# Performance work log

Hardware: AMD Instinct MI355X
Metric: run time of the kernel (lower is better)

## Reference

```python
import jax, jax.numpy as jnp
import numpy as np


def setup_inputs() -> dict:
    key = jax.random.key(0)
    ks = jax.random.split(key, 4)
    B, T, M, E, F = 4, 2048, 1024, 8, 4096
    hidden_states = jax.random.normal(ks[0], (B, T, M), dtype=jnp.float32)
    wg = jax.random.normal(ks[1], (M, E), dtype=jnp.float32) * (1.0 / np.sqrt(M))
    w1 = jax.random.normal(ks[2], (E, M, F), dtype=jnp.float32) * (1.0 / np.sqrt(M))
    b1 = jnp.zeros((E, F), dtype=jnp.float32)
    w2 = jax.random.normal(ks[3], (E, F, M), dtype=jnp.float32) * (1.0 / np.sqrt(F))
    b2 = jnp.zeros((E, M), dtype=jnp.float32)
    return {"hidden_states": hidden_states, "wg": wg, "w1": w1, "b1": b1, "w2": w2, "b2": b2}


def reference(hidden_states, wg, w1, b1, w2, b2):
    B, T, M = hidden_states.shape
    E = wg.shape[1]
    S = B * T
    MIN_CAPACITY = 4
    C = max((S + E - 1) // E, MIN_CAPACITY)  # capacity_factor = 1 (static)

    x = hidden_states.reshape(S, M)  # [S, M]

    # --- top-1 gating (deepspeed TopKGate, noisy=None, use_rts=False) ---
    logits = x @ wg                                  # [S, E]
    gates = jax.nn.softmax(logits, axis=-1)          # [S, E]
    idx = jnp.argmax(gates, axis=-1)                 # [S]
    mask1 = jax.nn.one_hot(idx, E, dtype=gates.dtype)  # [S, E]
    # aux loss (computed before capacity drop)
    l_aux = jnp.sum(gates.mean(0) * mask1.mean(0)) * E
    # position of each token within its expert's queue
    locations1 = jnp.cumsum(mask1, axis=0) - 1.0     # [S, E]
    mask1 = mask1 * (locations1 < C)                 # drop overflow tokens
    gates1_s = jnp.sum(gates * mask1, axis=1)        # [S]
    loc_s = jnp.sum(locations1 * mask1, axis=1).astype(jnp.int32)  # [S]
    loc_sc = jax.nn.one_hot(loc_s, C, dtype=gates.dtype)           # [S, C]

    combine_weights = jnp.einsum('se,sc->sec', gates1_s[:, None] * mask1, loc_sc)  # [S,E,C]
    dispatch_mask = (combine_weights > 0).astype(x.dtype)

    # --- dispatch ---
    dispatched = jnp.einsum('sec,sm->ecm', dispatch_mask, x)  # [E, C, M]

    # --- expert FFN (grouped GEMM) ---
    h = jax.nn.gelu(jnp.einsum('ecm,emf->ecf', dispatched, w1) + b1[:, None, :])
    expert_out = jnp.einsum('ecf,efm->ecm', h, w2) + b2[:, None, :]  # [E, C, M]

    # --- combine ---
    out = jnp.einsum('sec,ecm->sm', combine_weights, expert_out)  # [S, M]
    return out.reshape(B, T, M)
```

## Files before the change

kernel.cpp:

```cpp
#include <hip/hip_runtime.h>
#include <hip/hip_bf16.h>
#include <math.h>

#define S_TOK 8192
#define M_DIM 1024
#define E_NUM 8
#define F_DIM 4096
#define CAP   1024

typedef short short8 __attribute__((ext_vector_type(8)));
typedef float f32x4 __attribute__((ext_vector_type(4)));
typedef unsigned short ushortx4 __attribute__((ext_vector_type(4)));

__device__ inline unsigned short f2bf(float f) {
    union { float f; unsigned int u; } v; v.f = f;
    unsigned int r = v.u + 0x7fffu + ((v.u >> 16) & 1u);
    return (unsigned short)(r >> 16);
}

__device__ inline float gelu_fast(float x) {
    float y = 0.7978845608028654f * (x + 0.044715f * x * x * x);
    if (y > 40.f) return x;
    float e = exp2f(2.8853900817779268f * y);
    return x * e / (e + 1.0f);
}

__device__ inline void gl_lds16(const void* g, void* l) {
    __builtin_amdgcn_global_load_lds(
        (const __attribute__((address_space(1))) unsigned int*)g,
        (__attribute__((address_space(3))) unsigned int*)l, 16, 0, 0);
}

__global__ __launch_bounds__(256) void gating_kernel(
    const float* __restrict__ x, const float* __restrict__ wg,
    int* __restrict__ idx, float* __restrict__ gate)
{
    int wid = threadIdx.x >> 6;
    int lane = threadIdx.x & 63;
    int s = blockIdx.x * 4 + wid;
    const float* xs = x + (size_t)s * M_DIM;

    double acc[E_NUM];
#pragma unroll
    for (int e = 0; e < E_NUM; e++) acc[e] = 0.0;

    for (int i = lane; i < M_DIM; i += 64) {
        float xv = xs[i];
        float4 wa = *(const float4*)(wg + (size_t)i * E_NUM);
        float4 wb = *(const float4*)(wg + (size_t)i * E_NUM + 4);
        acc[0] += (double)xv * (double)wa.x;
        acc[1] += (double)xv * (double)wa.y;
        acc[2] += (double)xv * (double)wa.z;
        acc[3] += (double)xv * (double)wa.w;
        acc[4] += (double)xv * (double)wb.x;
        acc[5] += (double)xv * (double)wb.y;
        acc[6] += (double)xv * (double)wb.z;
        acc[7] += (double)xv * (double)wb.w;
    }
#pragma unroll
    for (int e = 0; e < E_NUM; e++) {
        double v = acc[e];
        for (int o = 32; o > 0; o >>= 1) v += __shfl_down(v, o, 64);
        acc[e] = v;
    }
    if (lane == 0) {
        double mx = acc[0]; int am = 0;
#pragma unroll
        for (int e = 1; e < E_NUM; e++) {
            if (acc[e] > mx) { mx = acc[e]; am = e; }
        }
        double se = 0.0;
#pragma unroll
        for (int e = 0; e < E_NUM; e++) se += exp(acc[e] - mx);
        idx[s] = am;
        gate[s] = (float)(1.0 / se);
    }
}

__global__ __launch_bounds__(1024) void scan_build(
    const int* __restrict__ idx, int* __restrict__ srcmap)
{
    __shared__ unsigned int sc[2][4][1024];
    int t = threadIdx.x;

    for (int i = t; i < E_NUM * CAP; i += 1024) srcmap[i] = -1;

    int eid[8];
    unsigned int cnt[E_NUM];
#pragma unroll
    for (int e = 0; e < E_NUM; e++) cnt[e] = 0;
#pragma unroll
    for (int i = 0; i < 8; i++) {
        int e = idx[t * 8 + i];
        eid[i] = e;
        cnt[e]++;
    }
    unsigned int pk[4];
#pragma unroll
    for (int i = 0; i < 4; i++) pk[i] = cnt[2 * i] | (cnt[2 * i + 1] << 16);
#pragma unroll
    for (int i = 0; i < 4; i++) sc[0][i][t] = pk[i];

    int buf = 0;
    for (int ofs = 1; ofs < 1024; ofs <<= 1) {
        __syncthreads();
        unsigned int v[4];
#pragma unroll
        for (int i = 0; i < 4; i++) {
            v[i] = sc[buf][i][t] + ((t >= ofs) ? sc[buf][i][t - ofs] : 0u);
            sc[buf ^ 1][i][t] = v[i];
        }
        buf ^= 1;
    }
    __syncthreads();
    unsigned int pos[E_NUM];
#pragma unroll
    for (int e = 0; e < E_NUM; e++) {
        unsigned int incl = (sc[buf][e >> 1][t] >> ((e & 1) * 16)) & 0xffffu;
        pos[e] = incl - cnt[e];
    }
#pragma unroll
    for (int i = 0; i < 8; i++) {
        int e = eid[i];
        unsigned int p = pos[e]++;
        if (p < CAP) srcmap[e * CAP + p] = t * 8 + i;
    }
}

__global__ __launch_bounds__(256) void dispatch_kernel(
    const float* __restrict__ x, const int* __restrict__ srcmap,
    unsigned short* __restrict__ A1)
{
    int slot = blockIdx.x;
    int s = srcmap[slot];
    int t = threadIdx.x;
    ushortx4 o;
    if (s >= 0) {
        float4 v = ((const float4*)(x + (size_t)s * M_DIM))[t];
        o[0] = f2bf(v.x); o[1] = f2bf(v.y); o[2] = f2bf(v.z); o[3] = f2bf(v.w);
    } else {
        o[0] = 0; o[1] = 0; o[2] = 0; o[3] = 0;
    }
    ((ushortx4*)(A1 + (size_t)slot * M_DIM))[t] = o;
}

__global__ __launch_bounds__(256) void transpose_cvt(
    const float* __restrict__ in, unsigned short* __restrict__ out, int R, int Cc)
{
    __shared__ float tile[32][33];
    int e = blockIdx.z;
    int br = blockIdx.y * 32, bc = blockIdx.x * 32;
    const float* ine = in + (size_t)e * R * Cc;
    unsigned short* oute = out + (size_t)e * R * Cc;
    int tx = threadIdx.x, ty = threadIdx.y;
#pragma unroll
    for (int i = 0; i < 32; i += 8)
        tile[ty + i][tx] = ine[(size_t)(br + ty + i) * Cc + (bc + tx)];
    __syncthreads();
#pragma unroll
    for (int i = 0; i < 32; i += 8)
        oute[(size_t)(bc + ty + i) * R + (br + tx)] = f2bf(tile[tx][ty + i]);
}

template <int MODE>
__global__ __launch_bounds__(256) void gemm_bf16(
    const unsigned short* __restrict__ A, const unsigned short* __restrict__ B,
    const float* __restrict__ bias, float* __restrict__ OutF,
    unsigned short* __restrict__ OutH,
    const int* __restrict__ srcmap, const float* __restrict__ gate,
    int K, int RA, int NB, int tilesM, int tilesN)
{
    __shared__ __align__(16) unsigned short As[2][128 * 32];
    __shared__ __align__(16) unsigned short Bs[2][128 * 32];

    int bid = blockIdx.x;
    int tpe = tilesM * tilesN;
    int e = bid / tpe;
    int rem = bid - e * tpe;
    int tm = rem / tilesN;
    int tn = rem - tm * tilesN;

    const unsigned short* Ae = A + ((size_t)e * RA + (size_t)tm * 128) * K;
    const unsigned short* Be = B + ((size_t)e * NB + (size_t)tn * 128) * K;

    int tid = threadIdx.x;
    int wid = tid >> 6, lane = tid & 63;
    int srow = wid * 32 + (lane >> 2);
    int schunk = (lane & 3) * 8;

    int fr = lane & 15, fk = (lane >> 4) * 8;
    int r0 = (wid >> 1) * 64, c0 = (wid & 1) * 64;

#define STAGE(bufi, kk) do {                                                  \
    const unsigned short* ga = Ae + (size_t)srow * K + (kk) + schunk;         \
    const unsigned short* gb = Be + (size_t)srow * K + (kk) + schunk;         \
    gl_lds16(ga,                 &As[bufi][srow * 32 + schunk]);              \
    gl_lds16(ga + (size_t)16 * K, &As[bufi][(srow + 16) * 32 + schunk]);      \
    gl_lds16(gb,                 &Bs[bufi][srow * 32 + schunk]);              \
    gl_lds16(gb + (size_t)16 * K, &Bs[bufi][(srow + 16) * 32 + schunk]);      \
} while (0)

    f32x4 acc[4][4];
#pragma unroll
    for (int i = 0; i < 4; i++)
#pragma unroll
        for (int j = 0; j < 4; j++) acc[i][j] = (f32x4){0.f, 0.f, 0.f, 0.f};

    STAGE(0, 0);
    asm volatile("s_waitcnt vmcnt(0)" ::: "memory");
    __syncthreads();

    int cur = 0;
    for (int k0 = 0; k0 < K; k0 += 32) {
        if (k0 + 32 < K) STAGE(cur ^ 1, k0 + 32);

        short8 a[4], b[4];
#pragma unroll
        for (int mi = 0; mi < 4; mi++)
            a[mi] = *(const short8*)&As[cur][(r0 + mi * 16 + fr) * 32 + fk];
#pragma unroll
        for (int ni = 0; ni < 4; ni++)
            b[ni] = *(const short8*)&Bs[cur][(c0 + ni * 16 + fr) * 32 + fk];
#pragma unroll
        for (int mi = 0; mi < 4; mi++)
#pragma unroll
            for (int ni = 0; ni < 4; ni++)
                acc[mi][ni] = __builtin_amdgcn_mfma_f32_16x16x32_bf16(
                    a[mi], b[ni], acc[mi][ni], 0, 0, 0);

        asm volatile("s_waitcnt vmcnt(0)" ::: "memory");
        __syncthreads();
        cur ^= 1;
    }
#undef STAGE

    int orow = (lane >> 4) * 4, ocol = lane & 15;
    if (MODE == 0) {
#pragma unroll
        for (int mi = 0; mi < 4; mi++) {
#pragma unroll
            for (int j = 0; j < 4; j++) {
                int r = tm * 128 + r0 + mi * 16 + orow + j;
                size_t rowbase = ((size_t)e * RA + r) * NB;
#pragma unroll
                for (int ni = 0; ni < 4; ni++) {
                    int c = tn * 128 + c0 + ni * 16 + ocol;
                    float v = acc[mi][ni][j] + bias[e * NB + c];
                    OutH[rowbase + c] = f2bf(gelu_fast(v));
                }
            }
        }
    } else {
#pragma unroll
        for (int mi = 0; mi < 4; mi++) {
#pragma unroll
            for (int j = 0; j < 4; j++) {
                int r = tm * 128 + r0 + mi * 16 + orow + j;
                int slot = e * RA + r;
                int s = srcmap[slot];
                if (s < 0) continue;
                float g = gate[s];
                size_t rowbase = (size_t)s * NB;
#pragma unroll
                for (int ni = 0; ni < 4; ni++) {
                    int c = tn * 128 + c0 + ni * 16 + ocol;
                    OutF[rowbase + c] = g * (acc[mi][ni][j] + bias[e * NB + c]);
                }
            }
        }
    }
}

extern "C" void kernel_launch(void* const* d_in, const int* in_sizes, int n_in,
                              void* d_out, int out_size, void* d_ws, size_t ws_size,
                              hipStream_t stream) {
    const float* x  = (const float*)d_in[0];
    const float* wg = (const float*)d_in[1];
    const float* w1 = (const float*)d_in[2];
    const float* b1 = (const float*)d_in[3];
    const float* w2 = (const float*)d_in[4];
    const float* b2 = (const float*)d_in[5];
    float* out = (float*)d_out;

    char* ws = (char*)d_ws;
    unsigned short* A1  = (unsigned short*)(ws);
    unsigned short* W1T = (unsigned short*)(ws + (size_t)(16u << 20));
    unsigned short* W2T = (unsigned short*)(ws + (size_t)(80u << 20));
    unsigned short* H   = (unsigned short*)(ws + (size_t)(144u << 20));
    int*   idx  = (int*)(ws + (size_t)(208u << 20));
    float* gate = (float*)(ws + (size_t)(208u << 20) + 32768);
    int*   srcm = (int*)(ws + (size_t)(208u << 20) + 65536);

    hipMemsetAsync(d_out, 0, (size_t)S_TOK * M_DIM * sizeof(float), stream);

    gating_kernel<<<S_TOK / 4, 256, 0, stream>>>(x, wg, idx, gate);
    scan_build<<<1, 1024, 0, stream>>>(idx, srcm);
    dispatch_kernel<<<E_NUM * CAP, 256, 0, stream>>>(x, srcm, A1);
    transpose_cvt<<<dim3(F_DIM / 32, M_DIM / 32, E_NUM), dim3(32, 8), 0, stream>>>(
        w1, W1T, M_DIM, F_DIM);
    transpose_cvt<<<dim3(M_DIM / 32, F_DIM / 32, E_NUM), dim3(32, 8), 0, stream>>>(
        w2, W2T, F_DIM, M_DIM);

    gemm_bf16<0><<<E_NUM * (CAP / 128) * (F_DIM / 128), 256, 0, stream>>>(
        A1, W1T, b1, nullptr, H, nullptr, nullptr,
        M_DIM, CAP, F_DIM, CAP / 128, F_DIM / 128);

    gemm_bf16<1><<<E_NUM * (CAP / 128) * (M_DIM / 128), 256, 0, stream>>>(
        H, W2T, b2, out, nullptr, srcm, gate,
        F_DIM, CAP, M_DIM, CAP / 128, M_DIM / 128);
}
```

Before: 375.8 us.

## Use 256x256 tiles with 4-stage LDS pipeline and split-K second GEMM

Replaces the 128x128 double-buffered bf16 GEMM with a 256x256 tile, 512-thread kernel that uses a 4-slot LDS ring with partial vmcnt waits, swizzled LDS layout, workgroup index swizzling, and MFMA priority hints. The second GEMM is split along K into two halves that write fp32 partials into workspace, and a new combine kernel sums the partials, adds bias, scales by gate and scatters to output. This aims to raise arithmetic intensity, hide load latency and fill the GPU for the smaller second GEMM, at the cost of an extra partial buffer round trip and one more launch. P overlays the W1T workspace region, which is safe only because W1T is no longer needed by then.

```diff
diff --git a/kernel.cpp b/kernel.cpp
--- a/kernel.cpp
+++ b/kernel.cpp
@@ -163,112 +163,157 @@
 }
 
 template <int MODE>
-__global__ __launch_bounds__(256) void gemm_bf16(
+__global__ __launch_bounds__(512, 1) void gemm256(
     const unsigned short* __restrict__ A, const unsigned short* __restrict__ B,
-    const float* __restrict__ bias, float* __restrict__ OutF,
-    unsigned short* __restrict__ OutH,
-    const int* __restrict__ srcmap, const float* __restrict__ gate,
-    int K, int RA, int NB, int tilesM, int tilesN)
-{
-    __shared__ __align__(16) unsigned short As[2][128 * 32];
-    __shared__ __align__(16) unsigned short Bs[2][128 * 32];
+    const float* __restrict__ bias, unsigned short* __restrict__ OutH,
+    float* __restrict__ OutP)
+{
+    constexpr int K   = (MODE == 0) ? 1024 : 4096;
+    constexpr int NB  = (MODE == 0) ? 4096 : 1024;
+    constexpr int NT  = (MODE == 0) ? 32 : 64;
+    constexpr int NWG = (MODE == 0) ? 512 : 256;
+
+    __shared__ unsigned short Asm[4 * 8192];
+    __shared__ unsigned short Bsm[4 * 8192];
 
     int bid = blockIdx.x;
-    int tpe = tilesM * tilesN;
-    int e = bid / tpe;
-    int rem = bid - e * tpe;
-    int tm = rem / tilesN;
-    int tn = rem - tm * tilesN;
-
-    const unsigned short* Ae = A + ((size_t)e * RA + (size_t)tm * 128) * K;
-    const unsigned short* Be = B + ((size_t)e * NB + (size_t)tn * 128) * K;
+    int swz = (bid & 7) * (NWG / 8) + (bid >> 3);
+    int e, tm, tn, ks, kOff;
+    if (MODE == 0) {
+        e = swz >> 6; int rem = swz & 63; tm = rem >> 4; tn = rem & 15; ks = 0; kOff = 0;
+    } else {
+        ks = swz & 1; int q = swz >> 1; e = q >> 4; int rem = q & 15;
+        tm = rem >> 2; tn = rem & 3; kOff = ks * 2048;
+    }
+
+    const unsigned short* Ae = A + ((size_t)e * CAP + (size_t)tm * 256) * K;
+    const unsigned short* Be = B + ((size_t)e * NB + (size_t)tn * 256) * K;
 
     int tid = threadIdx.x;
     int wid = tid >> 6, lane = tid & 63;
-    int srow = wid * 32 + (lane >> 2);
-    int schunk = (lane & 3) * 8;
-
-    int fr = lane & 15, fk = (lane >> 4) * 8;
-    int r0 = (wid >> 1) * 64, c0 = (wid & 1) * 64;
-
-#define STAGE(bufi, kk) do {                                                  \
-    const unsigned short* ga = Ae + (size_t)srow * K + (kk) + schunk;         \
-    const unsigned short* gb = Be + (size_t)srow * K + (kk) + schunk;         \
-    gl_lds16(ga,                 &As[bufi][srow * 32 + schunk]);              \
-    gl_lds16(ga + (size_t)16 * K, &As[bufi][(srow + 16) * 32 + schunk]);      \
-    gl_lds16(gb,                 &Bs[bufi][srow * 32 + schunk]);              \
-    gl_lds16(gb + (size_t)16 * K, &Bs[bufi][(srow + 16) * 32 + schunk]);      \
-} while (0)
-
-    f32x4 acc[4][4];
-#pragma unroll
-    for (int i = 0; i < 4; i++)
+    int wm = wid >> 2, wn = wid & 3;
+    int fr = lane & 15, kq = lane >> 4;
+    int swc = ((kq ^ ((fr >> 1) & 3)) << 3);
+
+    int rr = tid >> 2;
+    int cg = (tid & 3) ^ ((rr >> 1) & 3);
+    const unsigned short* srcA0 = Ae + (size_t)rr * K + kOff + cg * 8;
+    const unsigned short* srcA1 = srcA0 + (size_t)128 * K;
+    const unsigned short* srcB0 = Be + (size_t)rr * K + kOff + cg * 8;
+    const unsigned short* srcB1 = srcB0 + (size_t)128 * K;
+    unsigned short* ldsA = Asm + wid * 512;
+    unsigned short* ldsB = Bsm + wid * 512;
+
+#define STG_A(t_) do { int sl_ = ((t_) & 3) * 8192; int kk_ = (t_) * 32;          \
+    gl_lds16(srcA0 + kk_, ldsA + sl_); gl_lds16(srcA1 + kk_, ldsA + sl_ + 4096); } while (0)
+#define STG_B(t_) do { int sl_ = ((t_) & 3) * 8192; int kk_ = (t_) * 32;          \
+    gl_lds16(srcB0 + kk_, ldsB + sl_); gl_lds16(srcB1 + kk_, ldsB + sl_ + 4096); } while (0)
+
+    f32x4 acc[8][4];
+#pragma unroll
+    for (int i = 0; i < 8; i++)
 #pragma unroll
         for (int j = 0; j < 4; j++) acc[i][j] = (f32x4){0.f, 0.f, 0.f, 0.f};
 
-    STAGE(0, 0);
-    asm volatile("s_waitcnt vmcnt(0)" ::: "memory");
-    __syncthreads();
-
-    int cur = 0;
-    for (int k0 = 0; k0 < K; k0 += 32) {
-        if (k0 + 32 < K) STAGE(cur ^ 1, k0 + 32);
-
+    STG_A(0); STG_B(0); STG_A(1); STG_B(1); STG_A(2); STG_B(2);
+
+    int arow = wm * 128 + fr;
+    int brow = wn * 64 + fr;
+
+    for (int t = 0; t < NT; ++t) {
+        int sl = (t & 3) * 8192;
+        int rem = NT - 1 - t;
+        if (rem > 1)       asm volatile("s_waitcnt vmcnt(8)" ::: "memory");
+        else if (rem == 1) asm volatile("s_waitcnt vmcnt(4)" ::: "memory");
+        else               asm volatile("s_waitcnt vmcnt(0)" ::: "memory");
+        asm volatile("s_barrier" ::: "memory");
+
+        if (t + 3 < NT) STG_A(t + 3);
         short8 a[4], b[4];
 #pragma unroll
         for (int mi = 0; mi < 4; mi++)
-            a[mi] = *(const short8*)&As[cur][(r0 + mi * 16 + fr) * 32 + fk];
+            a[mi] = *(const short8*)&Asm[sl + (arow + mi * 16) * 32 + swc];
 #pragma unroll
         for (int ni = 0; ni < 4; ni++)
-            b[ni] = *(const short8*)&Bs[cur][(c0 + ni * 16 + fr) * 32 + fk];
+            b[ni] = *(const short8*)&Bsm[sl + (brow + ni * 16) * 32 + swc];
+        __builtin_amdgcn_s_setprio(1);
 #pragma unroll
         for (int mi = 0; mi < 4; mi++)
 #pragma unroll
             for (int ni = 0; ni < 4; ni++)
                 acc[mi][ni] = __builtin_amdgcn_mfma_f32_16x16x32_bf16(
                     a[mi], b[ni], acc[mi][ni], 0, 0, 0);
-
-        asm volatile("s_waitcnt vmcnt(0)" ::: "memory");
-        __syncthreads();
-        cur ^= 1;
-    }
-#undef STAGE
-
-    int orow = (lane >> 4) * 4, ocol = lane & 15;
+        __builtin_amdgcn_s_setprio(0);
+
+        if (t + 3 < NT) STG_B(t + 3);
+#pragma unroll
+        for (int mi = 0; mi < 4; mi++)
+            a[mi] = *(const short8*)&Asm[sl + (arow + (mi + 4) * 16) * 32 + swc];
+        __builtin_amdgcn_s_setprio(1);
+#pragma unroll
+        for (int mi = 0; mi < 4; mi++)
+#pragma unroll
+            for (int ni = 0; ni < 4; ni++)
+                acc[mi + 4][ni] = __builtin_amdgcn_mfma_f32_16x16x32_bf16(
+                    a[mi], b[ni], acc[mi + 4][ni], 0, 0, 0);
+        __builtin_amdgcn_s_setprio(0);
+    }
+#undef STG_A
+#undef STG_B
+
+    int orow = kq * 4, ocol = fr;
+    int cbase = tn * 256 + wn * 64;
     if (MODE == 0) {
-#pragma unroll
-        for (int mi = 0; mi < 4; mi++) {
+        float bv[4];
+#pragma unroll
+        for (int ni = 0; ni < 4; ni++) bv[ni] = bias[e * NB + cbase + ni * 16 + ocol];
+#pragma unroll
+        for (int mi = 0; mi < 8; mi++) {
 #pragma unroll
             for (int j = 0; j < 4; j++) {
-                int r = tm * 128 + r0 + mi * 16 + orow + j;
-                size_t rowbase = ((size_t)e * RA + r) * NB;
-#pragma unroll
-                for (int ni = 0; ni < 4; ni++) {
-                    int c = tn * 128 + c0 + ni * 16 + ocol;
-                    float v = acc[mi][ni][j] + bias[e * NB + c];
-                    OutH[rowbase + c] = f2bf(gelu_fast(v));
-                }
+                int r = tm * 256 + wm * 128 + mi * 16 + orow + j;
+                size_t rowbase = ((size_t)e * CAP + r) * NB + cbase;
+#pragma unroll
+                for (int ni = 0; ni < 4; ni++)
+                    OutH[rowbase + ni * 16 + ocol] = f2bf(gelu_fast(acc[mi][ni][j] + bv[ni]));
             }
         }
     } else {
-#pragma unroll
-        for (int mi = 0; mi < 4; mi++) {
+        float* OP = OutP + (size_t)ks * S_TOK * M_DIM;
+#pragma unroll
+        for (int mi = 0; mi < 8; mi++) {
 #pragma unroll
             for (int j = 0; j < 4; j++) {
-                int r = tm * 128 + r0 + mi * 16 + orow + j;
-                int slot = e * RA + r;
-                int s = srcmap[slot];
-                if (s < 0) continue;
-                float g = gate[s];
-                size_t rowbase = (size_t)s * NB;
-#pragma unroll
-                for (int ni = 0; ni < 4; ni++) {
-                    int c = tn * 128 + c0 + ni * 16 + ocol;
-                    OutF[rowbase + c] = g * (acc[mi][ni][j] + bias[e * NB + c]);
-                }
+                int r = tm * 256 + wm * 128 + mi * 16 + orow + j;
+                size_t rowbase = ((size_t)e * CAP + r) * NB + cbase;
+#pragma unroll
+                for (int ni = 0; ni < 4; ni++)
+                    OP[rowbase + ni * 16 + ocol] = acc[mi][ni][j];
             }
         }
     }
+}
+
+__global__ __launch_bounds__(256) void combine_kernel(
+    const float* __restrict__ P, const int* __restrict__ srcmap,
+    const float* __restrict__ gate, const float* __restrict__ b2,
+    float* __restrict__ out)
+{
+    int r = blockIdx.x;
+    int s = srcmap[r];
+    if (s < 0) return;
+    int e = r >> 10;
+    float g = gate[s];
+    int t = threadIdx.x;
+    float4 p0 = ((const float4*)P)[r * 256 + t];
+    float4 p1 = ((const float4*)(P + (size_t)S_TOK * M_DIM))[r * 256 + t];
+    float4 bb = ((const float4*)b2)[e * 256 + t];
+    float4 o;
+    o.x = g * (p0.x + p1.x + bb.x);
+    o.y = g * (p0.y + p1.y + bb.y);
+    o.z = g * (p0.z + p1.z + bb.z);
+    o.w = g * (p0.w + p1.w + bb.w);
+    ((float4*)out)[s * 256 + t] = o;
 }
 
 extern "C" void kernel_launch(void* const* d_in, const int* in_sizes, int n_in,
@@ -285,6 +330,7 @@
     char* ws = (char*)d_ws;
     unsigned short* A1  = (unsigned short*)(ws);
     unsigned short* W1T = (unsigned short*)(ws + (size_t)(16u << 20));
+    float*          P   = (float*)(ws + (size_t)(16u << 20));
     unsigned short* W2T = (unsigned short*)(ws + (size_t)(80u << 20));
     unsigned short* H   = (unsigned short*)(ws + (size_t)(144u << 20));
     int*   idx  = (int*)(ws + (size_t)(208u << 20));
@@ -301,11 +347,9 @@
     transpose_cvt<<<dim3(M_DIM / 32, F_DIM / 32, E_NUM), dim3(32, 8), 0, stream>>>(
         w2, W2T, F_DIM, M_DIM);
 
-    gemm_bf16<0><<<E_NUM * (CAP / 128) * (F_DIM / 128), 256, 0, stream>>>(
-        A1, W1T, b1, nullptr, H, nullptr, nullptr,
-        M_DIM, CAP, F_DIM, CAP / 128, F_DIM / 128);
-
-    gemm_bf16<1><<<E_NUM * (CAP / 128) * (M_DIM / 128), 256, 0, stream>>>(
-        H, W2T, b2, out, nullptr, srcm, gate,
-        F_DIM, CAP, M_DIM, CAP / 128, M_DIM / 128);
-}
+    gemm256<0><<<512, 512, 0, stream>>>(A1, W1T, b1, H, nullptr);
+
+    gemm256<1><<<256, 512, 0, stream>>>(H, W2T, nullptr, nullptr, P);
+
+    combine_kernel<<<E_NUM * CAP, 256, 0, stream>>>(P, srcm, gate, b2, out);
+}
```

New measurement: 341.8 us. 1.1x faster.

## Rewrite expert GEMMs with larger tiles, swizzled LDS and staged epilogue

Applied to the files above, without the earlier changes.

Replaces the 128x128x32 bf16 GEMM with a 512-thread kernel using 256x256 (FFN1) or 128x256 (FFN2) tiles and a K-step of 64. LDS rows get an XOR swizzle to avoid bank conflicts, and blocks are remapped for cache locality. MFMA issue is bracketed with setprio, and the FFN1 epilogue writes through LDS so global stores are vectorised. The goal is more data reuse per tile and fewer barriers per K; the cost is higher register and LDS pressure, which may lower occupancy.

```diff
diff --git a/kernel.cpp b/kernel.cpp
--- a/kernel.cpp
+++ b/kernel.cpp
@@ -163,109 +163,163 @@
 }
 
 template <int MODE>
-__global__ __launch_bounds__(256) void gemm_bf16(
+__global__ __launch_bounds__(512) void gemm256(
     const unsigned short* __restrict__ A, const unsigned short* __restrict__ B,
-    const float* __restrict__ bias, float* __restrict__ OutF,
-    unsigned short* __restrict__ OutH,
-    const int* __restrict__ srcmap, const float* __restrict__ gate,
-    int K, int RA, int NB, int tilesM, int tilesN)
-{
-    __shared__ __align__(16) unsigned short As[2][128 * 32];
-    __shared__ __align__(16) unsigned short Bs[2][128 * 32];
+    const float* __restrict__ bias, unsigned short* __restrict__ OutH,
+    float* __restrict__ OutF, const int* __restrict__ srcmap,
+    const float* __restrict__ gate)
+{
+    constexpr int K    = (MODE == 0) ? 1024 : 4096;
+    constexpr int NB   = (MODE == 0) ? 4096 : 1024;
+    constexpr int BM   = (MODE == 0) ? 256 : 128;
+    constexpr int NT   = K / 64;
+    constexpr int NWG  = (MODE == 0) ? 512 : 256;
+    constexpr int AI   = BM / 64;
+    constexpr int MI   = BM / 32;
+    constexpr int ASLOT = BM * 64;
+    constexpr int BBASE = BM * 128;
+
+    __shared__ __align__(16) unsigned short LDS[BBASE + 32768];
 
     int bid = blockIdx.x;
-    int tpe = tilesM * tilesN;
-    int e = bid / tpe;
-    int rem = bid - e * tpe;
-    int tm = rem / tilesN;
-    int tn = rem - tm * tilesN;
-
-    const unsigned short* Ae = A + ((size_t)e * RA + (size_t)tm * 128) * K;
-    const unsigned short* Be = B + ((size_t)e * NB + (size_t)tn * 128) * K;
-
-    int tid = threadIdx.x;
-    int wid = tid >> 6, lane = tid & 63;
-    int srow = wid * 32 + (lane >> 2);
-    int schunk = (lane & 3) * 8;
-
-    int fr = lane & 15, fk = (lane >> 4) * 8;
-    int r0 = (wid >> 1) * 64, c0 = (wid & 1) * 64;
-
-#define STAGE(bufi, kk) do {                                                  \
-    const unsigned short* ga = Ae + (size_t)srow * K + (kk) + schunk;         \
-    const unsigned short* gb = Be + (size_t)srow * K + (kk) + schunk;         \
-    gl_lds16(ga,                 &As[bufi][srow * 32 + schunk]);              \
-    gl_lds16(ga + (size_t)16 * K, &As[bufi][(srow + 16) * 32 + schunk]);      \
-    gl_lds16(gb,                 &Bs[bufi][srow * 32 + schunk]);              \
-    gl_lds16(gb + (size_t)16 * K, &Bs[bufi][(srow + 16) * 32 + schunk]);      \
+    int swz = (bid & 7) * (NWG / 8) + (bid >> 3);
+    int e, tm, tn;
+    if (MODE == 0) { e = swz >> 6; int r = swz & 63; tm = r >> 4; tn = r & 15; }
+    else           { e = swz >> 5; int r = swz & 31; tm = r >> 2; tn = r & 3; }
+
+    const unsigned short* Ae = A + ((size_t)e * CAP + (size_t)tm * BM) * K;
+    const unsigned short* Be = B + ((size_t)e * NB + (size_t)tn * 256) * K;
+
+    int tid = threadIdx.x, w = tid >> 6, lane = tid & 63;
+    int wm = w >> 2, wn = w & 3;
+    int fr = lane & 15, kq = lane >> 4;
+
+    const unsigned short* srcA[4]; int dA[4];
+#pragma unroll
+    for (int i = 0; i < AI; i++) {
+        int ks = i & 1;
+        int rb = (AI == 4) ? (w * 32 + (i >> 1) * 16) : (w * 16);
+        int row = rb + (lane >> 2);
+        int logc = (lane & 3) ^ ((row >> 1) & 3);
+        srcA[i] = Ae + (size_t)row * K + ks * 32 + logc * 8;
+        dA[i] = ks * (BM * 32) + rb * 32;
+    }
+    const unsigned short* srcB[4]; int dB[4];
+#pragma unroll
+    for (int i = 0; i < 4; i++) {
+        int ks = i & 1;
+        int rb = w * 32 + (i >> 1) * 16;
+        int row = rb + (lane >> 2);
+        int logc = (lane & 3) ^ ((row >> 1) & 3);
+        srcB[i] = Be + (size_t)row * K + ks * 32 + logc * 8;
+        dB[i] = ks * 8192 + rb * 32;
+    }
+
+#define STAGE(sl, t_) do { int k0_ = (t_) * 64;                                   \
+    gl_lds16(srcA[0] + k0_, &LDS[(sl) * ASLOT + dA[0]]);                          \
+    gl_lds16(srcA[1] + k0_, &LDS[(sl) * ASLOT + dA[1]]);                          \
+    if (AI == 4) {                                                                \
+        gl_lds16(srcA[2] + k0_, &LDS[(sl) * ASLOT + dA[2]]);                      \
+        gl_lds16(srcA[3] + k0_, &LDS[(sl) * ASLOT + dA[3]]);                      \
+    }                                                                             \
+    gl_lds16(srcB[0] + k0_, &LDS[BBASE + (sl) * 16384 + dB[0]]);                  \
+    gl_lds16(srcB[1] + k0_, &LDS[BBASE + (sl) * 16384 + dB[1]]);                  \
+    gl_lds16(srcB[2] + k0_, &LDS[BBASE + (sl) * 16384 + dB[2]]);                  \
+    gl_lds16(srcB[3] + k0_, &LDS[BBASE + (sl) * 16384 + dB[3]]);                  \
 } while (0)
 
-    f32x4 acc[4][4];
-#pragma unroll
-    for (int i = 0; i < 4; i++)
+    int aoff = (kq ^ ((fr >> 1) & 3)) * 8;
+    int arowb = (wm * (BM / 2) + fr) * 32 + aoff;
+    int browb = BBASE + (wn * 64 + fr) * 32 + aoff;
+
+    f32x4 acc[MI][4];
+#pragma unroll
+    for (int i = 0; i < MI; i++)
 #pragma unroll
         for (int j = 0; j < 4; j++) acc[i][j] = (f32x4){0.f, 0.f, 0.f, 0.f};
 
     STAGE(0, 0);
     asm volatile("s_waitcnt vmcnt(0)" ::: "memory");
-    __syncthreads();
+    __builtin_amdgcn_s_barrier();
 
     int cur = 0;
-    for (int k0 = 0; k0 < K; k0 += 32) {
-        if (k0 + 32 < K) STAGE(cur ^ 1, k0 + 32);
-
-        short8 a[4], b[4];
-#pragma unroll
-        for (int mi = 0; mi < 4; mi++)
-            a[mi] = *(const short8*)&As[cur][(r0 + mi * 16 + fr) * 32 + fk];
-#pragma unroll
-        for (int ni = 0; ni < 4; ni++)
-            b[ni] = *(const short8*)&Bs[cur][(c0 + ni * 16 + fr) * 32 + fk];
-#pragma unroll
-        for (int mi = 0; mi < 4; mi++)
-#pragma unroll
-            for (int ni = 0; ni < 4; ni++)
-                acc[mi][ni] = __builtin_amdgcn_mfma_f32_16x16x32_bf16(
-                    a[mi], b[ni], acc[mi][ni], 0, 0, 0);
-
-        asm volatile("s_waitcnt vmcnt(0)" ::: "memory");
-        __syncthreads();
+    for (int t = 0; t < NT; ++t) {
+        if (t + 1 < NT) STAGE(cur ^ 1, t + 1);
+
+        int as = cur * ASLOT, bs = cur * 16384;
+        short8 b[4][2];
+#pragma unroll
+        for (int ni = 0; ni < 4; ni++) {
+            b[ni][0] = *(const short8*)&LDS[bs + browb + ni * 512];
+            b[ni][1] = *(const short8*)&LDS[bs + browb + ni * 512 + 8192];
+        }
+#pragma unroll
+        for (int mh = 0; mh < MI / 4; ++mh) {
+            short8 a[4][2];
+#pragma unroll
+            for (int m2 = 0; m2 < 4; m2++) {
+                a[m2][0] = *(const short8*)&LDS[as + arowb + (mh * 4 + m2) * 512];
+                a[m2][1] = *(const short8*)&LDS[as + arowb + (mh * 4 + m2) * 512 + BM * 32];
+            }
+            __builtin_amdgcn_s_setprio(1);
+#pragma unroll
+            for (int m2 = 0; m2 < 4; m2++)
+#pragma unroll
+                for (int ni = 0; ni < 4; ni++) {
+                    acc[mh * 4 + m2][ni] = __builtin_amdgcn_mfma_f32_16x16x32_bf16(
+                        a[m2][0], b[ni][0], acc[mh * 4 + m2][ni], 0, 0, 0);
+                    acc[mh * 4 + m2][ni] = __builtin_amdgcn_mfma_f32_16x16x32_bf16(
+                        a[m2][1], b[ni][1], acc[mh * 4 + m2][ni], 0, 0, 0);
+                }
+            __builtin_amdgcn_s_setprio(0);
+        }
+
+        if (t + 1 < NT) asm volatile("s_waitcnt vmcnt(0)" ::: "memory");
+        __builtin_amdgcn_s_barrier();
         cur ^= 1;
     }
 #undef STAGE
 
-    int orow = (lane >> 4) * 4, ocol = lane & 15;
+    int cbase = tn * 256 + wn * 64;
     if (MODE == 0) {
-#pragma unroll
-        for (int mi = 0; mi < 4; mi++) {
+        float bv[4];
+#pragma unroll
+        for (int ni = 0; ni < 4; ni++) bv[ni] = bias[e * NB + cbase + ni * 16 + fr];
+#pragma unroll
+        for (int mi = 0; mi < MI; mi++) {
 #pragma unroll
             for (int j = 0; j < 4; j++) {
-                int r = tm * 128 + r0 + mi * 16 + orow + j;
-                size_t rowbase = ((size_t)e * RA + r) * NB;
+                int lrow = wm * 128 + mi * 16 + kq * 4 + j;
 #pragma unroll
                 for (int ni = 0; ni < 4; ni++) {
-                    int c = tn * 128 + c0 + ni * 16 + ocol;
-                    float v = acc[mi][ni][j] + bias[e * NB + c];
-                    OutH[rowbase + c] = f2bf(gelu_fast(v));
+                    int lcol = wn * 64 + ni * 16 + fr;
+                    LDS[lrow * 256 + lcol] = f2bf(gelu_fast(acc[mi][ni][j] + bv[ni]));
                 }
             }
         }
+        __syncthreads();
+        int row = tid >> 1, seg = tid & 1;
+        const short8* sp = (const short8*)&LDS[row * 256 + seg * 128];
+        short8* dp = (short8*)&OutH[((size_t)(e * CAP + tm * 256 + row)) * (size_t)NB
+                                    + tn * 256 + seg * 128];
+#pragma unroll
+        for (int i = 0; i < 16; i++) dp[i] = sp[i];
     } else {
-#pragma unroll
-        for (int mi = 0; mi < 4; mi++) {
+        float bv[4];
+#pragma unroll
+        for (int ni = 0; ni < 4; ni++) bv[ni] = bias[e * NB + cbase + ni * 16 + fr];
+#pragma unroll
+        for (int mi = 0; mi < MI; mi++) {
 #pragma unroll
             for (int j = 0; j < 4; j++) {
-                int r = tm * 128 + r0 + mi * 16 + orow + j;
-                int slot = e * RA + r;
-                int s = srcmap[slot];
+                int r = tm * BM + wm * (BM / 2) + mi * 16 + kq * 4 + j;
+                int s = srcmap[e * CAP + r];
                 if (s < 0) continue;
                 float g = gate[s];
-                size_t rowbase = (size_t)s * NB;
-#pragma unroll
-                for (int ni = 0; ni < 4; ni++) {
-                    int c = tn * 128 + c0 + ni * 16 + ocol;
-                    OutF[rowbase + c] = g * (acc[mi][ni][j] + bias[e * NB + c]);
-                }
+                float* ob = OutF + (size_t)s * NB + cbase;
+#pragma unroll
+                for (int ni = 0; ni < 4; ni++)
+                    ob[ni * 16 + fr] = g * (acc[mi][ni][j] + bv[ni]);
             }
         }
     }
@@ -301,11 +355,7 @@
     transpose_cvt<<<dim3(M_DIM / 32, F_DIM / 32, E_NUM), dim3(32, 8), 0, stream>>>(
         w2, W2T, F_DIM, M_DIM);
 
-    gemm_bf16<0><<<E_NUM * (CAP / 128) * (F_DIM / 128), 256, 0, stream>>>(
-        A1, W1T, b1, nullptr, H, nullptr, nullptr,
-        M_DIM, CAP, F_DIM, CAP / 128, F_DIM / 128);
-
-    gemm_bf16<1><<<E_NUM * (CAP / 128) * (M_DIM / 128), 256, 0, stream>>>(
-        H, W2T, b2, out, nullptr, srcm, gate,
-        F_DIM, CAP, M_DIM, CAP / 128, M_DIM / 128);
-}
+    gemm256<0><<<512, 512, 0, stream>>>(A1, W1T, b1, H, nullptr, nullptr, nullptr);
+
+    gemm256<1><<<256, 512, 0, stream>>>(H, W2T, b2, nullptr, out, srcm, gate);
+}
```

New measurement: 354.3 us. 5.7% less time.

## Rework expert GEMMs with K=64 tiles, XOR-swizzled LDS, block swizzle, staged epilogue

Applied to the files above, without the earlier changes.

Both expert GEMMs now use a templated kernel with compile-time shapes. Each stage loads a K=64 slice instead of K=32, halving the number of barriers per tile. LDS uses an XOR-swizzled layout to avoid bank conflicts. Block indices are remapped so neighbouring workgroups share operand tiles, and MFMA blocks run under raised s_setprio. The first GEMM stages its GELU output through LDS to write coalesced 16-byte rows, and the second GEMM hoists bias loads. LDS per block doubles to 64 KB, and launch_bounds requests 2 waves per SIMD, which may limit occupancy.

```diff
diff --git a/kernel.cpp b/kernel.cpp
--- a/kernel.cpp
+++ b/kernel.cpp
@@ -163,42 +163,63 @@
 }
 
 template <int MODE>
-__global__ __launch_bounds__(256) void gemm_bf16(
+__global__ __launch_bounds__(256, 2) void gemm128(
     const unsigned short* __restrict__ A, const unsigned short* __restrict__ B,
-    const float* __restrict__ bias, float* __restrict__ OutF,
-    unsigned short* __restrict__ OutH,
-    const int* __restrict__ srcmap, const float* __restrict__ gate,
-    int K, int RA, int NB, int tilesM, int tilesN)
-{
-    __shared__ __align__(16) unsigned short As[2][128 * 32];
-    __shared__ __align__(16) unsigned short Bs[2][128 * 32];
+    const float* __restrict__ bias, unsigned short* __restrict__ OutH,
+    float* __restrict__ OutF, const int* __restrict__ srcmap,
+    const float* __restrict__ gate)
+{
+    constexpr int K   = (MODE == 0) ? 1024 : 4096;
+    constexpr int NB  = (MODE == 0) ? 4096 : 1024;
+    constexpr int NT  = K / 64;
+    constexpr int TM  = 8;
+    constexpr int TN  = NB / 128;
+    constexpr int NWG = E_NUM * TM * TN;
+
+    __shared__ __align__(16) unsigned short LA[2][8192];
+    __shared__ __align__(16) unsigned short LB[2][8192];
 
     int bid = blockIdx.x;
-    int tpe = tilesM * tilesN;
-    int e = bid / tpe;
-    int rem = bid - e * tpe;
-    int tm = rem / tilesN;
-    int tn = rem - tm * tilesN;
-
-    const unsigned short* Ae = A + ((size_t)e * RA + (size_t)tm * 128) * K;
+    int swz = (bid & 7) * (NWG / 8) + (bid >> 3);
+    int e   = swz / (TM * TN);
+    int rem = swz % (TM * TN);
+    int tn  = rem / TM;
+    int tm  = rem % TM;
+
+    const unsigned short* Ae = A + ((size_t)e * CAP + (size_t)tm * 128) * K;
     const unsigned short* Be = B + ((size_t)e * NB + (size_t)tn * 128) * K;
 
-    int tid = threadIdx.x;
-    int wid = tid >> 6, lane = tid & 63;
-    int srow = wid * 32 + (lane >> 2);
-    int schunk = (lane & 3) * 8;
-
-    int fr = lane & 15, fk = (lane >> 4) * 8;
-    int r0 = (wid >> 1) * 64, c0 = (wid & 1) * 64;
-
-#define STAGE(bufi, kk) do {                                                  \
-    const unsigned short* ga = Ae + (size_t)srow * K + (kk) + schunk;         \
-    const unsigned short* gb = Be + (size_t)srow * K + (kk) + schunk;         \
-    gl_lds16(ga,                 &As[bufi][srow * 32 + schunk]);              \
-    gl_lds16(ga + (size_t)16 * K, &As[bufi][(srow + 16) * 32 + schunk]);      \
-    gl_lds16(gb,                 &Bs[bufi][srow * 32 + schunk]);              \
-    gl_lds16(gb + (size_t)16 * K, &Bs[bufi][(srow + 16) * 32 + schunk]);      \
+    int tid = threadIdx.x, w = tid >> 6, lane = tid & 63;
+    int wm = w >> 1, wn = w & 1;
+    int fr = lane & 15, kq = lane >> 4;
+    int r0 = wm * 64, c0 = wn * 64;
+
+    int lr = lane >> 3;
+    int lc = (lane & 7) ^ lr;
+    const unsigned short* gA[4]; const unsigned short* gB[4]; int dL[4];
+#pragma unroll
+    for (int i = 0; i < 4; i++) {
+        int rb = w * 32 + i * 8;
+        gA[i] = Ae + (size_t)(rb + lr) * K + lc * 8;
+        gB[i] = Be + (size_t)(rb + lr) * K + lc * 8;
+        dL[i] = rb * 64;
+    }
+
+#define STAGE(bf, t_) do { int k0_ = (t_) * 64;                      \
+    gl_lds16(gA[0] + k0_, &LA[bf][dL[0]]);                           \
+    gl_lds16(gA[1] + k0_, &LA[bf][dL[1]]);                           \
+    gl_lds16(gA[2] + k0_, &LA[bf][dL[2]]);                           \
+    gl_lds16(gA[3] + k0_, &LA[bf][dL[3]]);                           \
+    gl_lds16(gB[0] + k0_, &LB[bf][dL[0]]);                           \
+    gl_lds16(gB[1] + k0_, &LB[bf][dL[1]]);                           \
+    gl_lds16(gB[2] + k0_, &LB[bf][dL[2]]);                           \
+    gl_lds16(gB[3] + k0_, &LB[bf][dL[3]]);                           \
 } while (0)
+
+    int sw0 = ((kq)     ^ (fr & 7)) * 8;
+    int sw1 = ((4 + kq) ^ (fr & 7)) * 8;
+    int aBase = (r0 + fr) * 64;
+    int bBase = (c0 + fr) * 64;
 
     f32x4 acc[4][4];
 #pragma unroll
@@ -208,64 +229,86 @@
 
     STAGE(0, 0);
     asm volatile("s_waitcnt vmcnt(0)" ::: "memory");
-    __syncthreads();
+    __builtin_amdgcn_s_barrier();
 
     int cur = 0;
-    for (int k0 = 0; k0 < K; k0 += 32) {
-        if (k0 + 32 < K) STAGE(cur ^ 1, k0 + 32);
-
-        short8 a[4], b[4];
-#pragma unroll
-        for (int mi = 0; mi < 4; mi++)
-            a[mi] = *(const short8*)&As[cur][(r0 + mi * 16 + fr) * 32 + fk];
+    for (int t = 0; t < NT; ++t) {
+        if (t + 1 < NT) STAGE(cur ^ 1, t + 1);
+
+        short8 a[4][2], b[4][2];
+#pragma unroll
+        for (int mi = 0; mi < 4; mi++) {
+            a[mi][0] = *(const short8*)&LA[cur][aBase + mi * 1024 + sw0];
+            a[mi][1] = *(const short8*)&LA[cur][aBase + mi * 1024 + sw1];
+        }
+#pragma unroll
+        for (int ni = 0; ni < 4; ni++) {
+            b[ni][0] = *(const short8*)&LB[cur][bBase + ni * 1024 + sw0];
+            b[ni][1] = *(const short8*)&LB[cur][bBase + ni * 1024 + sw1];
+        }
+        __builtin_amdgcn_s_setprio(1);
+#pragma unroll
+        for (int ks = 0; ks < 2; ks++)
+#pragma unroll
+            for (int mi = 0; mi < 4; mi++)
+#pragma unroll
+                for (int ni = 0; ni < 4; ni++)
+                    acc[mi][ni] = __builtin_amdgcn_mfma_f32_16x16x32_bf16(
+                        a[mi][ks], b[ni][ks], acc[mi][ni], 0, 0, 0);
+        __builtin_amdgcn_s_setprio(0);
+
+        if (t + 1 < NT) asm volatile("s_waitcnt vmcnt(0)" ::: "memory");
+        __builtin_amdgcn_s_barrier();
+        cur ^= 1;
+    }
+#undef STAGE
+
+    if (MODE == 0) {
+        __syncthreads();
+        unsigned short* R = (unsigned short*)LA;
+        float bv[4];
 #pragma unroll
         for (int ni = 0; ni < 4; ni++)
-            b[ni] = *(const short8*)&Bs[cur][(c0 + ni * 16 + fr) * 32 + fk];
-#pragma unroll
-        for (int mi = 0; mi < 4; mi++)
-#pragma unroll
-            for (int ni = 0; ni < 4; ni++)
-                acc[mi][ni] = __builtin_amdgcn_mfma_f32_16x16x32_bf16(
-                    a[mi], b[ni], acc[mi][ni], 0, 0, 0);
-
-        asm volatile("s_waitcnt vmcnt(0)" ::: "memory");
-        __syncthreads();
-        cur ^= 1;
-    }
-#undef STAGE
-
-    int orow = (lane >> 4) * 4, ocol = lane & 15;
-    if (MODE == 0) {
+            bv[ni] = bias[e * NB + tn * 128 + c0 + ni * 16 + fr];
 #pragma unroll
         for (int mi = 0; mi < 4; mi++) {
 #pragma unroll
             for (int j = 0; j < 4; j++) {
-                int r = tm * 128 + r0 + mi * 16 + orow + j;
-                size_t rowbase = ((size_t)e * RA + r) * NB;
+                int row = r0 + mi * 16 + kq * 4 + j;
 #pragma unroll
                 for (int ni = 0; ni < 4; ni++) {
-                    int c = tn * 128 + c0 + ni * 16 + ocol;
-                    float v = acc[mi][ni][j] + bias[e * NB + c];
-                    OutH[rowbase + c] = f2bf(gelu_fast(v));
+                    int col = c0 + ni * 16 + fr;
+                    R[row * 128 + (((col >> 3) ^ (row & 7)) << 3) + (col & 7)] =
+                        f2bf(gelu_fast(acc[mi][ni][j] + bv[ni]));
                 }
             }
         }
+        __syncthreads();
+        int row = tid >> 1, seg = tid & 1;
+        size_t gb = ((size_t)(e * CAP + tm * 128 + row)) * NB + tn * 128 + seg * 64;
+#pragma unroll
+        for (int i = 0; i < 8; i++) {
+            int chunk = seg * 8 + i;
+            *(short8*)&OutH[gb + i * 8] =
+                *(const short8*)&R[row * 128 + ((chunk ^ (row & 7)) << 3)];
+        }
     } else {
+        float bv[4];
+#pragma unroll
+        for (int ni = 0; ni < 4; ni++)
+            bv[ni] = bias[e * NB + tn * 128 + c0 + ni * 16 + fr];
 #pragma unroll
         for (int mi = 0; mi < 4; mi++) {
 #pragma unroll
             for (int j = 0; j < 4; j++) {
-                int r = tm * 128 + r0 + mi * 16 + orow + j;
-                int slot = e * RA + r;
-                int s = srcmap[slot];
+                int r = tm * 128 + r0 + mi * 16 + kq * 4 + j;
+                int s = srcmap[e * CAP + r];
                 if (s < 0) continue;
                 float g = gate[s];
-                size_t rowbase = (size_t)s * NB;
-#pragma unroll
-                for (int ni = 0; ni < 4; ni++) {
-                    int c = tn * 128 + c0 + ni * 16 + ocol;
-                    OutF[rowbase + c] = g * (acc[mi][ni][j] + bias[e * NB + c]);
-                }
+                float* ob = OutF + (size_t)s * NB + tn * 128 + c0;
+#pragma unroll
+                for (int ni = 0; ni < 4; ni++)
+                    ob[ni * 16 + fr] = g * (acc[mi][ni][j] + bv[ni]);
             }
         }
     }
@@ -301,11 +344,7 @@
     transpose_cvt<<<dim3(M_DIM / 32, F_DIM / 32, E_NUM), dim3(32, 8), 0, stream>>>(
         w2, W2T, F_DIM, M_DIM);
 
-    gemm_bf16<0><<<E_NUM * (CAP / 128) * (F_DIM / 128), 256, 0, stream>>>(
-        A1, W1T, b1, nullptr, H, nullptr, nullptr,
-        M_DIM, CAP, F_DIM, CAP / 128, F_DIM / 128);
-
-    gemm_bf16<1><<<E_NUM * (CAP / 128) * (M_DIM / 128), 256, 0, stream>>>(
-        H, W2T, b2, out, nullptr, srcm, gate,
-        F_DIM, CAP, M_DIM, CAP / 128, M_DIM / 128);
-}
+    gemm128<0><<<2048, 256, 0, stream>>>(A1, W1T, b1, H, nullptr, nullptr, nullptr);
+
+    gemm128<1><<<512, 256, 0, stream>>>(H, W2T, b2, nullptr, out, srcm, gate);
+}
```

Measured after the change: 361.0 us. 3.9% less time.
